# Kernel tuning notes

Hardware: AMD Instinct MI355X
Metric: run time of the kernel (lower is better)

## Reference

```python
import jax, jax.numpy as jnp
import numpy as np

INF = 1e6  # stands in for +infinity in the distance transform (fp32-safe when squared)


def _edt(sites):
    """Exact Euclidean distance to the nearest True pixel.
    sites: bool [N, H, W] -> float32 [N, H, W].
    Pass 1: exact 1D distance along width via min-plus cumulative scans.
    Pass 2: lower envelope over rows, d2[y] = min_y' (g[y']^2 + (y-y')^2),
    computed row-by-row with lax.map to avoid an [N,H,W,H] intermediate.
    """
    N, H, W = sites.shape
    pen = jnp.where(sites, 0.0, INF).astype(jnp.float32)  # 0 at sites, INF elsewhere
    xs = jnp.arange(W, dtype=jnp.float32)
    # d_fwd[i] = min_{j<=i} (i - j + pen[j]);  d_bwd[i] = min_{j>=i} (j - i + pen[j])
    fwd = xs + jax.lax.cummin(pen - xs, axis=2)
    bwd = -xs + jax.lax.cummin(pen + xs, axis=2, reverse=True)
    g = jnp.minimum(fwd, bwd)  # exact 1D distance along width
    g2 = g * g
    ys = jnp.arange(H, dtype=jnp.float32)

    def row_min(y):
        # min over source row y' of g2[:, y', :] + (y - y')^2  -> [N, W]
        return jnp.min(g2 + ((y - ys) ** 2)[None, :, None], axis=1)

    d2 = jax.lax.map(row_min, ys)  # [H, N, W]
    return jnp.sqrt(jnp.transpose(d2, (1, 0, 2)))


def _phi(mask):
    """Signed level-set function: -dist_inside on foreground, +dist_outside on background.
    mask: bool [B, H, W]. Images with empty foreground get all-zero phi (as in the torch code).
    """
    sites = jnp.concatenate([~mask, mask], axis=0)  # nearest-background / nearest-foreground
    d = _edt(sites)
    B = mask.shape[0]
    din, dout = d[:B], d[B:]
    phi = jnp.where(mask, -din, dout)
    phi = jnp.where(jnp.abs(phi) > 1e5, 0.0, phi)  # guard degenerate (no-site) cases
    any_fg = jnp.any(mask, axis=(1, 2))
    return jnp.where(any_fg[:, None, None], phi, 0.0)


def setup_inputs() -> dict:
    key = jax.random.key(0)
    k1, k2 = jax.random.split(key)
    predictions = jax.random.normal(k1, (16, 1, 512, 512), dtype=jnp.float32)
    targets = jax.random.randint(k2, (16, 1, 512, 512), 0, 2, dtype=jnp.int32)
    return {"predictions": predictions, "targets": targets}


def reference(predictions, targets):
    alpha = 0.01      # initial_alpha, 'rebalance' schedule at epoch 0
    smooth = 1e-6
    p = jax.nn.sigmoid(predictions)
    t = targets.astype(jnp.float32)
    # Dice loss
    inter = jnp.sum(p * t)
    dice = 1.0 - (2.0 * inter + smooth) / (jnp.sum(p) + jnp.sum(t) + smooth)
    # Boundary loss
    phi = _phi(targets[:, 0].astype(bool))[:, None]  # [B,1,H,W]
    boundary = jnp.mean(phi * p)
    return (1.0 - alpha) * dice + alpha * boundary
```

## Files before the change

### kernel.cpp

```cpp
#include <hip/hip_runtime.h>


#define HH 512
#define WW 512
#define BH 16
#define HALO 16
#define TR 48
#define NT 512
#define NBLK 512
#define NGRP 4

__device__ float fallback_exact(const int* __restrict__ t, int n, int y, int x,
                                bool fg, float m2) {
    const int* tn = t + (n << 18);
    for (int yy = 0; yy < HH; ++yy) {
        float dy = (float)(yy - y);
        float dy2 = dy * dy;
        if (dy2 >= m2) continue;
        const int* row = tn + (yy << 9);
        int lim = (int)sqrtf(m2 - dy2);
        if (lim > WW) lim = WW;
        for (int dx = 0; dx <= lim; ++dx) {
            bool hit = false;
            int xl = x - dx, xr = x + dx;
            if (xl >= 0) { int v = row[xl]; hit = fg ? (v == 0) : (v != 0); }
            if (!hit && xr < WW) { int v = row[xr]; hit = fg ? (v == 0) : (v != 0); }
            if (hit) {
                float c = fmaf((float)dx, (float)dx, dy2);
                if (c < m2) m2 = c;
                break;
            }
        }
    }
    return m2;
}

__global__ __launch_bounds__(NT, 4) void edt_fused(const int* __restrict__ t,
                                                   const float* __restrict__ pred,
                                                   double* __restrict__ partials) {
    __shared__ unsigned long long msk[TR][8];
    __shared__ unsigned char gb[TR][WW];
    __shared__ double sred[8][4];

    const int n     = blockIdx.x >> 5;
    const int y0    = (blockIdx.x & 31) << 4;
    const int rbase = y0 - HALO;
    const int wave  = threadIdx.x >> 6;
    const int lane  = threadIdx.x & 63;
    const int x0    = lane << 3;

    for (int rr = wave; rr < TR; rr += 8) {
        const int gy = rbase + rr;
        if (gy < 0 || gy >= HH) continue;
        const int4* tp = (const int4*)(t + (n << 18) + (gy << 9) + x0);
        int4 ta = tp[0], tb = tp[1];
        unsigned int byte = 0;
        byte |= (unsigned int)(ta.x != 0) << 0;
        byte |= (unsigned int)(ta.y != 0) << 1;
        byte |= (unsigned int)(ta.z != 0) << 2;
        byte |= (unsigned int)(ta.w != 0) << 3;
        byte |= (unsigned int)(tb.x != 0) << 4;
        byte |= (unsigned int)(tb.y != 0) << 5;
        byte |= (unsigned int)(tb.z != 0) << 6;
        byte |= (unsigned int)(tb.w != 0) << 7;
        ((unsigned char*)&msk[rr][0])[lane] = (unsigned char)byte;
    }
    __syncthreads();

    {
        const int s  = (lane - 3) << 3;
        const int sh = s & 63;
        const int j0 = s >> 6;
        unsigned long long V = ~0ull;
        if (s < 0)   V &= (~0ull) << (-s);
        if (s > 448) V &= (~0ull) >> (s - 448);

        for (int rr = wave; rr < TR; rr += 8) {
            const int gy = rbase + rr;
            unsigned long long pk;
            if (gy < 0 || gy >= HH) {
                pk = 0xBFBFBFBFBFBFBFBFull;
            } else {
                unsigned long long w0 = (j0 >= 0) ? msk[rr][j0] : 0ull;
                unsigned long long w1 = (j0 < 7) ? msk[rr][j0 + 1] : 0ull;
                unsigned long long win = sh ? ((w0 >> sh) | (w1 << (64 - sh))) : w0;
                pk = 0ull;
#pragma unroll
                for (int i = 0; i < 8; ++i) {
                    const int c = 24 + i;
                    unsigned int b = (unsigned int)(win >> c) & 1u;
                    unsigned long long mm = (b ? ~win : win) & V;
                    unsigned long long lo = mm & ((1ull << c) - 1ull);
                    unsigned long long hi = mm >> (c + 1);
                    int dl = lo ? (c - 63 + __builtin_clzll(lo)) : 64;
                    int dr = hi ? (1 + (int)__builtin_ctzll(hi)) : 64;
                    int g = min(min(dl, dr), 63);
                    pk |= ((unsigned long long)((b << 6) | (unsigned int)g)) << (i * 8);
                }
            }
            *((unsigned long long*)&gb[rr][x0]) = pk;
        }
    }
    __syncthreads();

    double s_b = 0.0, s_p = 0.0, s_i = 0.0;
    int s_t = 0;

#pragma unroll 1
    for (int grp = 0; grp < NGRP; ++grp) {
        const int pid = (grp * NT + threadIdx.x) << 2;
        const int yl  = pid >> 9;
        const int x   = pid & 511;
        const int r   = yl + HALO;

        const float4 p4 = *((const float4*)(pred + (n << 18) + ((y0 + yl) << 9) + x));
        const float pv[4] = {p4.x, p4.y, p4.z, p4.w};

        const unsigned int ow = *((const unsigned int*)&gb[r][x]);
        int  m2[4], wc[4];
        bool fg[4];
        int  mx = 0;
#pragma unroll
        for (int j = 0; j < 4; ++j) {
            unsigned int bj  = (ow >> (8 * j)) & 255u;
            unsigned int cls = bj >> 6;
            int gg = (int)(bj & 63u);
            fg[j] = (cls == 1u);
            wc[j] = fg[j] ? 0 : 1;
            m2[j] = gg * gg;
            mx = max(mx, m2[j]);
        }

        for (int k = 1; k <= HALO; ++k) {
            const int k2 = k * k;
            if (k2 >= mx) break;
            const unsigned int bd = *((const unsigned int*)&gb[r - k][x]);
            const unsigned int bu = *((const unsigned int*)&gb[r + k][x]);
            mx = 0;
#pragma unroll
            for (int j = 0; j < 4; ++j) {
                if (k2 < m2[j]) {
                    unsigned int dj = (bd >> (8 * j)) & 255u;
                    unsigned int uj = (bu >> (8 * j)) & 255u;
                    int a = ((int)(dj >> 6) == wc[j]) ? 0 : (int)(dj & 63u);
                    int b = ((int)(uj >> 6) == wc[j]) ? 0 : (int)(uj & 63u);
                    m2[j] = min(m2[j], min(a * a + k2, b * b + k2));
                }
                mx = max(mx, m2[j]);
            }
        }

        float df[4];
#pragma unroll
        for (int j = 0; j < 4; ++j) df[j] = sqrtf((float)m2[j]);

        if (mx > 289) {
#pragma unroll
            for (int j = 0; j < 4; ++j)
                if (m2[j] > 289) {
                    float fm2 = fallback_exact(t, n, y0 + yl, x + j, fg[j], 1.0e12f);
                    df[j] = sqrtf(fm2);
                }
        }

#pragma unroll
        for (int j = 0; j < 4; ++j) {
            float p = 1.0f / (1.0f + expf(-pv[j]));
            float phi = fg[j] ? -df[j] : df[j];
            if (df[j] > 1.0e4f) phi = 0.0f;
            s_b += (double)(phi * p);
            s_p += (double)p;
            if (fg[j]) { s_i += (double)p; s_t += 1; }
        }
    }
    double s_tt = (double)s_t;

#pragma unroll
    for (int off = 32; off > 0; off >>= 1) {
        s_b  += __shfl_xor(s_b,  off, 64);
        s_p  += __shfl_xor(s_p,  off, 64);
        s_i  += __shfl_xor(s_i,  off, 64);
        s_tt += __shfl_xor(s_tt, off, 64);
    }
    if (lane == 0) {
        sred[wave][0] = s_b; sred[wave][1] = s_p; sred[wave][2] = s_i; sred[wave][3] = s_tt;
    }
    __syncthreads();
    if (threadIdx.x == 0) {
        double* dst = partials + (size_t)blockIdx.x * 4;
#pragma unroll
        for (int c = 0; c < 4; ++c) {
            double acc = 0.0;
#pragma unroll
            for (int wv = 0; wv < 8; ++wv) acc += sred[wv][c];
            dst[c] = acc;
        }
    }
}

__global__ __launch_bounds__(512) void finalize_loss(const double* __restrict__ partials,
                                                     float* __restrict__ out) {
    const int wave = threadIdx.x >> 6;
    const int lane = threadIdx.x & 63;
    const double* src = partials + (size_t)threadIdx.x * 4;
    double s0 = src[0], s1 = src[1], s2 = src[2], s3 = src[3];
#pragma unroll
    for (int off = 32; off > 0; off >>= 1) {
        s0 += __shfl_xor(s0, off, 64);
        s1 += __shfl_xor(s1, off, 64);
        s2 += __shfl_xor(s2, off, 64);
        s3 += __shfl_xor(s3, off, 64);
    }
    __shared__ double red[8][4];
    if (lane == 0) { red[wave][0] = s0; red[wave][1] = s1; red[wave][2] = s2; red[wave][3] = s3; }
    __syncthreads();
    if (threadIdx.x == 0) {
        double sb = 0.0, sp = 0.0, si = 0.0, st = 0.0;
#pragma unroll
        for (int wv = 0; wv < 8; ++wv) {
            sb += red[wv][0]; sp += red[wv][1]; si += red[wv][2]; st += red[wv][3];
        }
        double dice = 1.0 - (2.0 * si + 1e-6) / (sp + st + 1e-6);
        double boundary = sb / (double)(16 * 512 * 512);
        out[0] = (float)(0.99 * dice + 0.01 * boundary);
    }
}

extern "C" void kernel_launch(void* const* d_in, const int* in_sizes, int n_in,
                              void* d_out, int out_size, void* d_ws, size_t ws_size,
                              hipStream_t stream) {
    const float* pred = (const float*)d_in[0];
    const int*   targ = (const int*)d_in[1];
    double* partials = (double*)d_ws;
    float* out = (float*)d_out;

    edt_fused<<<NBLK, NT, 0, stream>>>(targ, pred, partials);
    finalize_loss<<<1, 512, 0, stream>>>(partials, out);
}
```

Measured before the change: 97.94 us.

## Shrink EDT halo to 8 rows and fuse final reduction via last-block atomic

Reduces the row halo from 16 to 8, so the shared tile holds 32 rows instead of 48, and lowers the fallback threshold to 81 so the exact global search covers pixels whose distance exceeds the halo. The separate finalize kernel is removed: each block atomically increments a counter, and the last block to arrive performs the global reduction. This cuts shared-memory staging and one kernel launch, but it adds a memset launch, and pixels farther than 9 pixels from their nearest opposite-class pixel now take the slow exact fallback. On the random test mask such pixels are essentially absent.

```diff
diff --git a/kernel.cpp b/kernel.cpp
--- a/kernel.cpp
+++ b/kernel.cpp
@@ -4,11 +4,12 @@
 #define HH 512
 #define WW 512
 #define BH 16
-#define HALO 16
-#define TR 48
+#define HALO 8
+#define TR 32
 #define NT 512
 #define NBLK 512
 #define NGRP 4
+#define T2MAX 81
 
 __device__ float fallback_exact(const int* __restrict__ t, int n, int y, int x,
                                 bool fg, float m2) {
@@ -37,10 +38,13 @@
 
 __global__ __launch_bounds__(NT, 4) void edt_fused(const int* __restrict__ t,
                                                    const float* __restrict__ pred,
-                                                   double* __restrict__ partials) {
+                                                   double* __restrict__ partials,
+                                                   unsigned int* __restrict__ count,
+                                                   float* __restrict__ out) {
     __shared__ unsigned long long msk[TR][8];
     __shared__ unsigned char gb[TR][WW];
     __shared__ double sred[8][4];
+    __shared__ int lastblk;
 
     const int n     = blockIdx.x >> 5;
     const int y0    = (blockIdx.x & 31) << 4;
@@ -154,10 +158,10 @@
 #pragma unroll
         for (int j = 0; j < 4; ++j) df[j] = sqrtf((float)m2[j]);
 
-        if (mx > 289) {
+        if (mx > T2MAX) {
 #pragma unroll
             for (int j = 0; j < 4; ++j)
-                if (m2[j] > 289) {
+                if (m2[j] > T2MAX) {
                     float fm2 = fallback_exact(t, n, y0 + yl, x + j, fg[j], 1.0e12f);
                     df[j] = sqrtf(fm2);
                 }
@@ -195,34 +199,35 @@
             for (int wv = 0; wv < 8; ++wv) acc += sred[wv][c];
             dst[c] = acc;
         }
-    }
-}
-
-__global__ __launch_bounds__(512) void finalize_loss(const double* __restrict__ partials,
-                                                     float* __restrict__ out) {
-    const int wave = threadIdx.x >> 6;
-    const int lane = threadIdx.x & 63;
-    const double* src = partials + (size_t)threadIdx.x * 4;
-    double s0 = src[0], s1 = src[1], s2 = src[2], s3 = src[3];
-#pragma unroll
-    for (int off = 32; off > 0; off >>= 1) {
-        s0 += __shfl_xor(s0, off, 64);
-        s1 += __shfl_xor(s1, off, 64);
-        s2 += __shfl_xor(s2, off, 64);
-        s3 += __shfl_xor(s3, off, 64);
-    }
-    __shared__ double red[8][4];
-    if (lane == 0) { red[wave][0] = s0; red[wave][1] = s1; red[wave][2] = s2; red[wave][3] = s3; }
-    __syncthreads();
-    if (threadIdx.x == 0) {
-        double sb = 0.0, sp = 0.0, si = 0.0, st = 0.0;
-#pragma unroll
-        for (int wv = 0; wv < 8; ++wv) {
-            sb += red[wv][0]; sp += red[wv][1]; si += red[wv][2]; st += red[wv][3];
-        }
-        double dice = 1.0 - (2.0 * si + 1e-6) / (sp + st + 1e-6);
-        double boundary = sb / (double)(16 * 512 * 512);
-        out[0] = (float)(0.99 * dice + 0.01 * boundary);
+        __threadfence();
+        unsigned int prev = atomicAdd(count, 1u);
+        lastblk = (prev == NBLK - 1u) ? 1 : 0;
+    }
+    __syncthreads();
+
+    if (lastblk) {
+        __threadfence();
+        const double* src = partials + (size_t)threadIdx.x * 4;
+        double r0 = src[0], r1 = src[1], r2 = src[2], r3 = src[3];
+#pragma unroll
+        for (int off = 32; off > 0; off >>= 1) {
+            r0 += __shfl_xor(r0, off, 64);
+            r1 += __shfl_xor(r1, off, 64);
+            r2 += __shfl_xor(r2, off, 64);
+            r3 += __shfl_xor(r3, off, 64);
+        }
+        if (lane == 0) { sred[wave][0] = r0; sred[wave][1] = r1; sred[wave][2] = r2; sred[wave][3] = r3; }
+        __syncthreads();
+        if (threadIdx.x == 0) {
+            double sb = 0.0, sp = 0.0, si = 0.0, st = 0.0;
+#pragma unroll
+            for (int wv = 0; wv < 8; ++wv) {
+                sb += sred[wv][0]; sp += sred[wv][1]; si += sred[wv][2]; st += sred[wv][3];
+            }
+            double dice = 1.0 - (2.0 * si + 1e-6) / (sp + st + 1e-6);
+            double boundary = sb / (double)(16 * 512 * 512);
+            out[0] = (float)(0.99 * dice + 0.01 * boundary);
+        }
     }
 }
 
@@ -232,8 +237,9 @@
     const float* pred = (const float*)d_in[0];
     const int*   targ = (const int*)d_in[1];
     double* partials = (double*)d_ws;
+    unsigned int* count = (unsigned int*)((char*)d_ws + 16384);
     float* out = (float*)d_out;
 
-    edt_fused<<<NBLK, NT, 0, stream>>>(targ, pred, partials);
-    finalize_loss<<<1, 512, 0, stream>>>(partials, out);
+    hipMemsetAsync(count, 0, sizeof(unsigned int), stream);
+    edt_fused<<<NBLK, NT, 0, stream>>>(targ, pred, partials, count, out);
 }
```

Result: no change. 99.83 us (+1.9%).
